# Optimization experiments

Hardware: AMD Instinct MI355X
Metric: run time of the kernel (lower is better)

The kernel has to match this reference:

```python
import jax, jax.numpy as jnp
import numpy as np

ALPHA = 0.2  # LeakyReLU negative slope
MASK_FILL = -9e15


def setup_inputs() -> dict:
    key = jax.random.key(0)
    k_x, k_adj, k_W, k_a = jax.random.split(key, 4)
    B, N, Fin, T, O = 8, 1024, 64, 8, 128
    x = jax.random.normal(k_x, (B, N, Fin, T), dtype=jnp.float32)
    adj = (jax.random.uniform(k_adj, (N, N)) < 0.05).astype(jnp.float32)
    adj = jnp.maximum(adj, jnp.eye(N, dtype=jnp.float32))
    W = jax.random.normal(k_W, (Fin, O), dtype=jnp.float32) * (1.414 * (6.0 / (Fin + O)) ** 0.5)
    a = jax.random.normal(k_a, (2 * O, 1), dtype=jnp.float32) * (1.414 * (6.0 / (2 * O + 1)) ** 0.5)
    return {"x": x, "adj": adj, "W": W, "a": a}


def reference(x, adj, W, a):
    # x: (B, N, Fin, T), adj: (N, N), W: (Fin, O), a: (2O, 1)
    O = W.shape[1]
    xt = jnp.transpose(x, (0, 3, 1, 2))                 # (B, T, N, Fin)
    Wh = jnp.einsum('btnf,fo->btno', xt, W)             # (B, T, N, O)
    a1 = a[:O, 0]                                       # (O,)
    a2 = a[O:, 0]                                       # (O,)
    Wh1 = Wh @ a1                                       # (B, T, N)
    Wh2 = Wh @ a2                                       # (B, T, N)
    e = Wh1[..., :, None] + Wh2[..., None, :]           # (B, T, N, N): e_ij = Wh1_i + Wh2_j
    e = jax.nn.leaky_relu(e, negative_slope=ALPHA)
    e = jnp.where(adj > 0, e, MASK_FILL)
    attn = jax.nn.softmax(e, axis=-1)                   # softmax over neighbors j (torch dim=1 on (N,N))
    # dropout on attention is identity at inference (training=False)
    h_prime = jnp.einsum('btij,btjo->btio', attn, Wh)   # (B, T, N, O)
    out = jnp.transpose(h_prime, (0, 2, 3, 1))          # (B, N, O, T)
    return jax.nn.elu(out)                              # concat=True -> ELU
```

## Files before the change

kernel.cpp:

```cpp
#include <hip/hip_runtime.h>
#include <math.h>
#include <stdint.h>

#define ALPHA 0.2f

typedef __attribute__((ext_vector_type(8)))  short bf16x8;
typedef __attribute__((ext_vector_type(4)))  float f32x4;
typedef __attribute__((ext_vector_type(16))) float f32x16;

__device__ __forceinline__ uint32_t pack_bf16(float a, float b) {
    return ((__float_as_uint(a) + 0x8000u) >> 16) |
           ((__float_as_uint(b) + 0x8000u) & 0xFFFF0000u);
}
__device__ __forceinline__ unsigned short bf16_1(float a) {
    return (unsigned short)((__float_as_uint(a) + 0x8000u) >> 16);
}

__global__ __launch_bounds__(256) void k_pre(const float* __restrict__ x,
                                             const float* __restrict__ W,
                                             const float* __restrict__ a,
                                             const float* __restrict__ adj,
                                             uint4* __restrict__ Whf,
                                             float* __restrict__ Wh1,
                                             float* __restrict__ Wh2,
                                             unsigned char* __restrict__ adjq) {
    __shared__ __attribute__((aligned(16))) unsigned short xbf[4 * 32 * 64];
    __shared__ __attribute__((aligned(16))) unsigned short Wbf[128 * 64];

    if (blockIdx.x >= 512) {
        int idx = (blockIdx.x - 512) * 256 + threadIdx.x;
        int i   = idx >> 7;
        int pos = idx & 127;
        const float4* a4 = (const float4*)adj + idx * 2;
        float4 v0 = a4[0], v1 = a4[1];
        unsigned int by = 0;
        by |= (v0.x > 0.f) ? 1u : 0u;
        by |= (v0.y > 0.f) ? 2u : 0u;
        by |= (v0.z > 0.f) ? 4u : 0u;
        by |= (v0.w > 0.f) ? 8u : 0u;
        by |= (v1.x > 0.f) ? 16u : 0u;
        by |= (v1.y > 0.f) ? 32u : 0u;
        by |= (v1.z > 0.f) ? 64u : 0u;
        by |= (v1.w > 0.f) ? 128u : 0u;
        adjq[(i << 7) + ((pos & 1) << 6) + (((pos >> 1) & 1) << 5) + (pos >> 2)] =
            (unsigned char)by;
        return;
    }

    const int tid  = threadIdx.x;
    const int b    = blockIdx.x & 7;
    const int jt32 = (blockIdx.x >> 3) & 31;
    const int th   = blockIdx.x >> 8;

    const float* xg = x + ((size_t)(b * 1024 + jt32 * 32) * 64) * 8 + th * 4;
    #pragma unroll
    for (int i = 0; i < 8; ++i) {
        int idx = tid + i * 256;
        int j   = idx >> 6;
        int f   = idx & 63;
        float4 v = *(const float4*)(xg + (size_t)(j * 64 + f) * 8);
        const int sw = ((j & 7) << 4);
        *(unsigned short*)((char*)xbf + ((((0 * 32 + j) * 64 + f) * 2) ^ sw)) = bf16_1(v.x);
        *(unsigned short*)((char*)xbf + ((((1 * 32 + j) * 64 + f) * 2) ^ sw)) = bf16_1(v.y);
        *(unsigned short*)((char*)xbf + ((((2 * 32 + j) * 64 + f) * 2) ^ sw)) = bf16_1(v.z);
        *(unsigned short*)((char*)xbf + ((((3 * 32 + j) * 64 + f) * 2) ^ sw)) = bf16_1(v.w);
    }
    const float4* Wg4 = (const float4*)W;
    #pragma unroll
    for (int i = 0; i < 8; ++i) {
        int idx = tid + i * 256;
        int fr  = idx >> 5;
        int o0  = (idx & 31) * 4;
        float4 v = Wg4[idx];
        #pragma unroll
        for (int c = 0; c < 4; ++c) {
            int o = o0 + c;
            *(unsigned short*)((char*)Wbf + (((o * 64 + fr) * 2) ^ ((o & 7) << 4))) =
                bf16_1((&v.x)[c]);
        }
    }
    __syncthreads();

    const int w   = tid >> 6;
    const int l   = tid & 63;
    const int col = l & 31;
    const int g   = l >> 5;
    const int t   = th * 4 + w;
    const int bt  = b * 8 + t;

    f32x16 acc[4];
    #pragma unroll
    for (int nt2 = 0; nt2 < 4; ++nt2)
        #pragma unroll
        for (int r = 0; r < 16; ++r) acc[nt2][r] = 0.f;

    #pragma unroll
    for (int kk = 0; kk < 4; ++kk) {
        union { uint4 u4; bf16x8 v8; } av;
        const int abyte = (((w * 32 + col) * 64 + kk * 16 + g * 8) * 2) ^ ((col & 7) << 4);
        av.u4 = *(const uint4*)((const char*)xbf + abyte);
        #pragma unroll
        for (int nt2 = 0; nt2 < 4; ++nt2) {
            union { uint4 u4; bf16x8 v8; } bv;
            const int o     = nt2 * 32 + col;
            const int bbyte = ((o * 64 + kk * 16 + g * 8) * 2) ^ ((o & 7) << 4);
            bv.u4 = *(const uint4*)((const char*)Wbf + bbyte);
            acc[nt2] = __builtin_amdgcn_mfma_f32_32x32x16_bf16(
                av.v8, bv.v8, acc[nt2], 0, 0, 0);
        }
    }

    float a1v[4], a2v[4];
    #pragma unroll
    for (int nt2 = 0; nt2 < 4; ++nt2) {
        a1v[nt2] = a[nt2 * 32 + col];
        a2v[nt2] = a[128 + nt2 * 32 + col];
    }
    #pragma unroll
    for (int reg = 0; reg < 16; ++reg) {
        float s1 = acc[0][reg] * a1v[0] + acc[1][reg] * a1v[1]
                 + acc[2][reg] * a1v[2] + acc[3][reg] * a1v[3];
        float s2 = acc[0][reg] * a2v[0] + acc[1][reg] * a2v[1]
                 + acc[2][reg] * a2v[2] + acc[3][reg] * a2v[3];
        #pragma unroll
        for (int off = 1; off < 32; off <<= 1) {
            s1 += __shfl_xor(s1, off);
            s2 += __shfl_xor(s2, off);
        }
        if (col == 0) {
            int j = jt32 * 32 + (reg & 3) + 8 * (reg >> 2) + 4 * g;
            Wh1[bt * 1024 + j] = s1;
            Wh2[bt * 1024 + j] = s2;
        }
    }

    #pragma unroll
    for (int nt2 = 0; nt2 < 4; ++nt2) {
        const uint32_t pk0 = pack_bf16(acc[nt2][0],  acc[nt2][1]);
        const uint32_t pk1 = pack_bf16(acc[nt2][2],  acc[nt2][3]);
        const uint32_t pk2 = pack_bf16(acc[nt2][4],  acc[nt2][5]);
        const uint32_t pk3 = pack_bf16(acc[nt2][6],  acc[nt2][7]);
        const uint32_t pk4 = pack_bf16(acc[nt2][8],  acc[nt2][9]);
        const uint32_t pk5 = pack_bf16(acc[nt2][10], acc[nt2][11]);
        const uint32_t pk6 = pack_bf16(acc[nt2][12], acc[nt2][13]);
        const uint32_t pk7 = pack_bf16(acc[nt2][14], acc[nt2][15]);
        const uint32_t xp0 = __shfl_xor(pk0, 32);
        const uint32_t xp1 = __shfl_xor(pk1, 32);
        const uint32_t xp2 = __shfl_xor(pk2, 32);
        const uint32_t xp3 = __shfl_xor(pk3, 32);
        const uint32_t xp4 = __shfl_xor(pk4, 32);
        const uint32_t xp5 = __shfl_xor(pk5, 32);
        const uint32_t xp6 = __shfl_xor(pk6, 32);
        const uint32_t xp7 = __shfl_xor(pk7, 32);
        const bool gh = (g != 0);

        uint4 s0, s1q;
        s0.x  = gh ? xp2 : pk0;
        s0.y  = gh ? xp3 : pk1;
        s0.z  = gh ? pk2 : xp0;
        s0.w  = gh ? pk3 : xp1;
        s1q.x = gh ? xp6 : pk4;
        s1q.y = gh ? xp7 : pk5;
        s1q.z = gh ? pk6 : xp4;
        s1q.w = gh ? pk7 : xp5;

        const size_t base = ((size_t)(bt * 4 + nt2) * 64 + jt32 * 2) * 64 + l;
        Whf[base]      = s0;
        Whf[base + 64] = s1q;
    }
}

__global__ __launch_bounds__(256) void k_agg(const uint4* __restrict__ Whf,
                                             const float* __restrict__ Wh1,
                                             const float* __restrict__ Wh2,
                                             const unsigned char* __restrict__ adjq,
                                             float* __restrict__ out) {
    __shared__ __attribute__((aligned(16))) uint4 bstage[2][1024];
    __shared__ __attribute__((aligned(16))) float efsE[1024];
    __shared__ __attribute__((aligned(16))) float efsF[1024];
    __shared__ float m2s[4];

    const int tid   = threadIdx.x;
    const int b     = blockIdx.x & 7;
    const int t     = (blockIdx.x >> 3) & 7;
    const int itile = blockIdx.x >> 6;
    const int bt    = b * 8 + t;
    const int i0    = itile * 128;

    const int w   = tid >> 6;
    const int l   = tid & 63;
    const int col = l & 31;
    const int g   = l >> 5;
    const int row = w * 32 + col;

    const uint4* plane = Whf + (size_t)bt * 16384;

    uint4 pf[4];
    #pragma unroll
    for (int f = 0; f < 4; ++f) pf[f] = plane[(w * 64 + f) * 64 + l];

    const uint4* ap = (const uint4*)(adjq + ((size_t)(i0 + row) << 7) + (g << 6));
    uint4 am[4];
    #pragma unroll
    for (int f = 0; f < 4; ++f) am[f] = ap[f];

    const float* wh2g = Wh2 + bt * 1024;
    float mx = -1e30f;
    #pragma unroll
    for (int rep = 0; rep < 4; ++rep) {
        int   j  = tid + rep * 256;
        float h2 = wh2g[j];
        efsE[j] = __expf(h2);
        efsF[j] = __expf(ALPHA * h2);
        mx = fmaxf(mx, h2);
    }
    #pragma unroll
    for (int off = 1; off < 64; off <<= 1) mx = fmaxf(mx, __shfl_xor(mx, off));
    if (l == 0) m2s[w] = mx;
    const float h1 = Wh1[bt * 1024 + i0 + row];

    #pragma unroll
    for (int f = 0; f < 4; ++f) bstage[0][(w * 4 + f) * 64 + l] = pf[f];
    __syncthreads();

    const float M2 = fmaxf(fmaxf(m2s[0], m2s[1]), fmaxf(m2s[2], m2s[3]));
    const float e0 = h1 + M2;
    const float mp = fmaxf(e0, ALPHA * e0);
    const float Af = __expf(h1 - mp);
    const float Bf = __expf(ALPHA * h1 - mp);

    f32x16 acc[4];
    #pragma unroll
    for (int nt2 = 0; nt2 < 4; ++nt2)
        #pragma unroll
        for (int r = 0; r < 16; ++r) acc[nt2][r] = 0.f;
    f32x16 accl;
    #pragma unroll
    for (int r = 0; r < 16; ++r) accl[r] = 0.f;

    bf16x8 ones;
    #pragma unroll
    for (int i = 0; i < 8; ++i) ones[i] = (short)0x3F80;

    #pragma unroll
    for (int v = 0; v < 16; ++v) {
        if (v + 1 < 16) {
            #pragma unroll
            for (int f = 0; f < 4; ++f)
                pf[f] = plane[(w * 64 + (v + 1) * 4 + f) * 64 + l];
        }

        #pragma unroll
        for (int ts = 0; ts < 4; ++ts) {
            const int jb = v * 64 + ts * 16 + g * 8;
            float4 E0 = *(const float4*)&efsE[jb];
            float4 E1 = *(const float4*)&efsE[jb + 4];
            float4 F0 = *(const float4*)&efsF[jb];
            float4 F1 = *(const float4*)&efsF[jb + 4];

            const int      pe = (ts & 1) * 32 + (v >> 1) * 4 + (v & 1) * 2 + (ts >> 1);
            const uint4    av = am[pe >> 4];
            const int      cc = (pe >> 2) & 3;
            const uint32_t cw = (cc == 0) ? av.x : (cc == 1) ? av.y
                               : (cc == 2) ? av.z : av.w;
            const uint32_t by = (cw >> ((pe & 3) * 8)) & 0xFFu;

            float p[8];
            p[0] = fmaxf(Af * E0.x, Bf * F0.x) * (float)((by >> 0) & 1u);
            p[1] = fmaxf(Af * E0.y, Bf * F0.y) * (float)((by >> 1) & 1u);
            p[2] = fmaxf(Af * E0.z, Bf * F0.z) * (float)((by >> 2) & 1u);
            p[3] = fmaxf(Af * E0.w, Bf * F0.w) * (float)((by >> 3) & 1u);
            p[4] = fmaxf(Af * E1.x, Bf * F1.x) * (float)((by >> 4) & 1u);
            p[5] = fmaxf(Af * E1.y, Bf * F1.y) * (float)((by >> 5) & 1u);
            p[6] = fmaxf(Af * E1.z, Bf * F1.z) * (float)((by >> 6) & 1u);
            p[7] = fmaxf(Af * E1.w, Bf * F1.w) * (float)((by >> 7) & 1u);

            union { uint32_t u32[4]; bf16x8 v8; } pk;
            #pragma unroll
            for (int r = 0; r < 4; ++r)
                pk.u32[r] = pack_bf16(p[2 * r], p[2 * r + 1]);

            #pragma unroll
            for (int nt2 = 0; nt2 < 4; ++nt2) {
                union { uint4 u4; bf16x8 v8; } br;
                br.u4 = bstage[v & 1][(nt2 * 4 + ts) * 64 + l];
                acc[nt2] = __builtin_amdgcn_mfma_f32_32x32x16_bf16(
                    pk.v8, br.v8, acc[nt2], 0, 0, 0);
            }
            accl = __builtin_amdgcn_mfma_f32_32x32x16_bf16(
                pk.v8, ones, accl, 0, 0, 0);
        }

        if (v + 1 < 16) {
            #pragma unroll
            for (int f = 0; f < 4; ++f)
                bstage[(v + 1) & 1][(w * 4 + f) * 64 + l] = pf[f];
        }
        __syncthreads();
    }

    float* og = out + ((size_t)(b * 1024 + i0 + w * 32)) * 1024 + t;
    #pragma unroll
    for (int reg = 0; reg < 16; ++reg) {
        const int   r    = (reg & 3) + 8 * (reg >> 2) + 4 * g;
        const float linv = 1.0f / accl[reg];
        #pragma unroll
        for (int nt2 = 0; nt2 < 4; ++nt2) {
            float vv = acc[nt2][reg] * linv;
            vv = vv > 0.f ? vv : __expf(vv) - 1.f;
            og[(size_t)r * 1024 + (nt2 * 32 + col) * 8] = vv;
        }
    }
}

extern "C" void kernel_launch(void* const* d_in, const int* in_sizes, int n_in,
                              void* d_out, int out_size, void* d_ws, size_t ws_size,
                              hipStream_t stream) {
    const float* x   = (const float*)d_in[0];
    const float* adj = (const float*)d_in[1];
    const float* W   = (const float*)d_in[2];
    const float* a   = (const float*)d_in[3];
    float* out = (float*)d_out;

    uint4*         Whf  = (uint4*)d_ws;
    float*         Wh1  = (float*)(Whf + 1048576);
    float*         Wh2  = Wh1 + 65536;
    unsigned char* adjq = (unsigned char*)(Wh2 + 65536);

    k_pre<<<1024, 256, 0, stream>>>(x, W, a, adj, Whf, Wh1, Wh2, adjq);
    k_agg<<<512, 256, 0, stream>>>(Whf, Wh1, Wh2, adjq, out);
}
```

Baseline: 135.1 us.

## Load MFMA B operands directly from global and drop LDS staging and barriers

Removes the double-buffered LDS staging of Wh fragments and the per-iteration __syncthreads. Each wave now loads its own B operands from global memory (L2-resident) with register ping-pong prefetch one slice ahead. The packed adjacency layout changes so each 16-column step reads one 32-bit word per iteration, and s_setprio wraps the MFMA bursts. In exchange, every wave reloads the whole plane from global/L2 instead of sharing it through LDS, and the main loop is no longer unrolled.

```diff
diff --git a/kernel.cpp b/kernel.cpp
--- a/kernel.cpp
+++ b/kernel.cpp
@@ -42,7 +42,7 @@
         by |= (v1.y > 0.f) ? 32u : 0u;
         by |= (v1.z > 0.f) ? 64u : 0u;
         by |= (v1.w > 0.f) ? 128u : 0u;
-        adjq[(i << 7) + ((pos & 1) << 6) + (((pos >> 1) & 1) << 5) + (pos >> 2)] =
+        adjq[(i << 7) + ((pos & 1) << 6) + ((pos >> 3) << 2) + ((pos >> 1) & 3)] =
             (unsigned char)by;
         return;
     }
@@ -170,12 +170,45 @@
     }
 }
 
+#define TSBODY(TS, QU, QV, NEXTSLOT)                                          \
+    {                                                                         \
+        _Pragma("unroll")                                                     \
+        for (int nt2 = 0; nt2 < 4; ++nt2)                                     \
+            QV[nt2].u4 = plane[(nt2 * 64 + (NEXTSLOT)) * 64 + l];             \
+        const int jb = v * 64 + (TS) * 16 + g * 8;                            \
+        float4 E0 = *(const float4*)&efsE[jb];                                \
+        float4 E1 = *(const float4*)&efsE[jb + 4];                            \
+        float4 F0 = *(const float4*)&efsF[jb];                                \
+        float4 F1 = *(const float4*)&efsF[jb + 4];                            \
+        const uint32_t by = (by32 >> ((TS) * 8)) & 0xFFu;                     \
+        float p[8];                                                           \
+        p[0] = fmaxf(Af * E0.x, Bf * F0.x) * (float)((by >> 0) & 1u);         \
+        p[1] = fmaxf(Af * E0.y, Bf * F0.y) * (float)((by >> 1) & 1u);         \
+        p[2] = fmaxf(Af * E0.z, Bf * F0.z) * (float)((by >> 2) & 1u);         \
+        p[3] = fmaxf(Af * E0.w, Bf * F0.w) * (float)((by >> 3) & 1u);         \
+        p[4] = fmaxf(Af * E1.x, Bf * F1.x) * (float)((by >> 4) & 1u);         \
+        p[5] = fmaxf(Af * E1.y, Bf * F1.y) * (float)((by >> 5) & 1u);         \
+        p[6] = fmaxf(Af * E1.z, Bf * F1.z) * (float)((by >> 6) & 1u);         \
+        p[7] = fmaxf(Af * E1.w, Bf * F1.w) * (float)((by >> 7) & 1u);         \
+        union { uint32_t u32[4]; bf16x8 v8; } pk;                             \
+        _Pragma("unroll")                                                     \
+        for (int r = 0; r < 4; ++r)                                           \
+            pk.u32[r] = pack_bf16(p[2 * r], p[2 * r + 1]);                    \
+        __builtin_amdgcn_s_setprio(1);                                        \
+        _Pragma("unroll")                                                     \
+        for (int nt2 = 0; nt2 < 4; ++nt2)                                     \
+            acc[nt2] = __builtin_amdgcn_mfma_f32_32x32x16_bf16(               \
+                pk.v8, QU[nt2].v8, acc[nt2], 0, 0, 0);                        \
+        accl = __builtin_amdgcn_mfma_f32_32x32x16_bf16(                       \
+            pk.v8, ones, accl, 0, 0, 0);                                      \
+        __builtin_amdgcn_s_setprio(0);                                        \
+    }
+
 __global__ __launch_bounds__(256) void k_agg(const uint4* __restrict__ Whf,
                                              const float* __restrict__ Wh1,
                                              const float* __restrict__ Wh2,
                                              const unsigned char* __restrict__ adjq,
                                              float* __restrict__ out) {
-    __shared__ __attribute__((aligned(16))) uint4 bstage[2][1024];
     __shared__ __attribute__((aligned(16))) float efsE[1024];
     __shared__ __attribute__((aligned(16))) float efsF[1024];
     __shared__ float m2s[4];
@@ -194,15 +227,7 @@
     const int row = w * 32 + col;
 
     const uint4* plane = Whf + (size_t)bt * 16384;
-
-    uint4 pf[4];
-    #pragma unroll
-    for (int f = 0; f < 4; ++f) pf[f] = plane[(w * 64 + f) * 64 + l];
-
-    const uint4* ap = (const uint4*)(adjq + ((size_t)(i0 + row) << 7) + (g << 6));
-    uint4 am[4];
-    #pragma unroll
-    for (int f = 0; f < 4; ++f) am[f] = ap[f];
+    const unsigned char* arow = adjq + ((size_t)(i0 + row) << 7) + (g << 6);
 
     const float* wh2g = Wh2 + bt * 1024;
     float mx = -1e30f;
@@ -218,9 +243,6 @@
     for (int off = 1; off < 64; off <<= 1) mx = fmaxf(mx, __shfl_xor(mx, off));
     if (l == 0) m2s[w] = mx;
     const float h1 = Wh1[bt * 1024 + i0 + row];
-
-    #pragma unroll
-    for (int f = 0; f < 4; ++f) bstage[0][(w * 4 + f) * 64 + l] = pf[f];
     __syncthreads();
 
     const float M2 = fmaxf(fmaxf(m2s[0], m2s[1]), fmaxf(m2s[2], m2s[3]));
@@ -242,61 +264,19 @@
     #pragma unroll
     for (int i = 0; i < 8; ++i) ones[i] = (short)0x3F80;
 
-    #pragma unroll
+    union qb { uint4 u4; bf16x8 v8; };
+    qb qX[4], qY[4];
+    #pragma unroll
+    for (int nt2 = 0; nt2 < 4; ++nt2)
+        qX[nt2].u4 = plane[(nt2 * 64 + 0) * 64 + l];
+
+    #pragma unroll 1
     for (int v = 0; v < 16; ++v) {
-        if (v + 1 < 16) {
-            #pragma unroll
-            for (int f = 0; f < 4; ++f)
-                pf[f] = plane[(w * 64 + (v + 1) * 4 + f) * 64 + l];
-        }
-
-        #pragma unroll
-        for (int ts = 0; ts < 4; ++ts) {
-            const int jb = v * 64 + ts * 16 + g * 8;
-            float4 E0 = *(const float4*)&efsE[jb];
-            float4 E1 = *(const float4*)&efsE[jb + 4];
-            float4 F0 = *(const float4*)&efsF[jb];
-            float4 F1 = *(const float4*)&efsF[jb + 4];
-
-            const int      pe = (ts & 1) * 32 + (v >> 1) * 4 + (v & 1) * 2 + (ts >> 1);
-            const uint4    av = am[pe >> 4];
-            const int      cc = (pe >> 2) & 3;
-            const uint32_t cw = (cc == 0) ? av.x : (cc == 1) ? av.y
-                               : (cc == 2) ? av.z : av.w;
-            const uint32_t by = (cw >> ((pe & 3) * 8)) & 0xFFu;
-
-            float p[8];
-            p[0] = fmaxf(Af * E0.x, Bf * F0.x) * (float)((by >> 0) & 1u);
-            p[1] = fmaxf(Af * E0.y, Bf * F0.y) * (float)((by >> 1) & 1u);
-            p[2] = fmaxf(Af * E0.z, Bf * F0.z) * (float)((by >> 2) & 1u);
-            p[3] = fmaxf(Af * E0.w, Bf * F0.w) * (float)((by >> 3) & 1u);
-            p[4] = fmaxf(Af * E1.x, Bf * F1.x) * (float)((by >> 4) & 1u);
-            p[5] = fmaxf(Af * E1.y, Bf * F1.y) * (float)((by >> 5) & 1u);
-            p[6] = fmaxf(Af * E1.z, Bf * F1.z) * (float)((by >> 6) & 1u);
-            p[7] = fmaxf(Af * E1.w, Bf * F1.w) * (float)((by >> 7) & 1u);
-
-            union { uint32_t u32[4]; bf16x8 v8; } pk;
-            #pragma unroll
-            for (int r = 0; r < 4; ++r)
-                pk.u32[r] = pack_bf16(p[2 * r], p[2 * r + 1]);
-
-            #pragma unroll
-            for (int nt2 = 0; nt2 < 4; ++nt2) {
-                union { uint4 u4; bf16x8 v8; } br;
-                br.u4 = bstage[v & 1][(nt2 * 4 + ts) * 64 + l];
-                acc[nt2] = __builtin_amdgcn_mfma_f32_32x32x16_bf16(
-                    pk.v8, br.v8, acc[nt2], 0, 0, 0);
-            }
-            accl = __builtin_amdgcn_mfma_f32_32x32x16_bf16(
-                pk.v8, ones, accl, 0, 0, 0);
-        }
-
-        if (v + 1 < 16) {
-            #pragma unroll
-            for (int f = 0; f < 4; ++f)
-                bstage[(v + 1) & 1][(w * 4 + f) * 64 + l] = pf[f];
-        }
-        __syncthreads();
+        const uint32_t by32 = *(const uint32_t*)(arow + v * 4);
+        TSBODY(0, qX, qY, v * 4 + 1)
+        TSBODY(1, qY, qX, v * 4 + 2)
+        TSBODY(2, qX, qY, v * 4 + 3)
+        TSBODY(3, qY, qX, ((v + 1) & 15) * 4)
     }
 
     float* og = out + ((size_t)(b * 1024 + i0 + w * 32)) * 1024 + t;
```

New measurement: 135.2 us. Within noise of the previous version (+0.1%).
